# Kernel optimization log

Measured on AMD Instinct MI355X. Metric: run time of the kernel, lower is better.

The kernel has to match this reference:

```python
import jax, jax.numpy as jnp
import numpy as np

R = 29          # GF_kernel_size_train
EPS = 1e-09     # loss_eps
SAMPLING = 8    # sampling_in_MSEloss
LAMBDA_TV = 0.1
LAMBDA_HESSIAN = 0.5
ISO = True      # isotropic_hessian
SIGMA = 1.0     # hessian_kernel_sigma (>0.5 -> generateHessianKernel, angle_offset=[0])


def _hessian_kernels():
    half = int(np.ceil(SIGMA * 6))
    t = np.linspace(-half, half, 2 * half + 1)
    X, Y = np.meshgrid(t, t, indexing='ij')
    g = np.exp(-(X ** 2 + Y ** 2) / (2 * SIGMA ** 2))
    dxx = (1.0 / (2 * np.pi * SIGMA ** 4)) * (X ** 2 / SIGMA ** 2 - 1) * g
    dxy = (1.0 / (2 * np.pi * SIGMA ** 6)) * (X * Y) * g
    dyy = dxx.T
    # Loss.__init__ unpacks generateHessianKernel's return (Gaussyy, Gaussxx, Gaussxy)
    # into (self.DGaussxx, self.DGaussyy, self.DGaussxy); angle_offset=[0] -> identity rotate.
    Gxx = dyy.astype(np.float32)[None, None]
    Gyy = dxx.astype(np.float32)[None, None]
    Gxy = dxy.astype(np.float32)[None, None]
    return jnp.asarray(Gxx), jnp.asarray(Gyy), jnp.asarray(Gxy)


def _conv(x, k):
    return jax.lax.conv_general_dilated(x, k, (1, 1), 'VALID',
                                        dimension_numbers=('NCHW', 'OIHW', 'NCHW'))


def _boxfilter(x, r):
    # F.pad(input, (r+1, r, r+1, r)) pads last two dims (left r+1, right r each)
    xp = jnp.pad(x, ((0, 0), (0, 0), (r + 1, r), (r + 1, r)))
    c = jnp.cumsum(xp, axis=3)
    d = c[:, :, :, 2 * r + 1:] - c[:, :, :, :-2 * r - 1]
    c2 = jnp.cumsum(d, axis=2)
    return c2[:, :, 2 * r + 1:, :] - c2[:, :, :-2 * r - 1, :]


def _guided_filter(x, y, r, eps):
    N = _boxfilter(jnp.ones_like(x), r)
    mean_x = _boxfilter(x, r) / N
    mean_y = _boxfilter(y, r) / N
    cov_xy = _boxfilter(x * y, r) / N - mean_x * mean_y
    var_x = _boxfilter(x * x, r) / N - mean_x * mean_x
    A = cov_xy / jnp.clip(var_x, EPS, None)
    b = mean_y - A * mean_x
    A = _boxfilter(A, r) / N
    b = _boxfilter(b, r) / N
    return A * x + b


def _tv(x, target, Dx, Dy):
    return jnp.abs(_conv(x, Dx)).sum() + jnp.abs(_conv(x - target, Dy)).sum()


def _hessian(x, target, Gxx, Gyy, Gxy):
    scale = 2.0 if ISO else 1.0
    return (jnp.abs(_conv(x, Gxx)).sum()
            + jnp.abs(_conv(x - target, Gyy)).sum()
            + (jnp.abs(_conv(x - target, Gxy)) * scale).sum())


def setup_inputs() -> dict:
    key = jax.random.key(0)
    ks = jax.random.split(key, 6)
    shape = (1, 1, 3072, 3072)
    Gxx, Gyy, Gxy = _hessian_kernels()
    return {
        'outputGNNraw': jax.random.normal(ks[0], shape, dtype=jnp.float32),
        'outputGNN': jax.random.normal(ks[1], shape, dtype=jnp.float32),
        'outputLR': jax.random.normal(ks[2], shape, dtype=jnp.float32),
        'smoothedTarget': jax.random.normal(ks[3], shape, dtype=jnp.float32),
        'targets': jax.random.normal(ks[4], shape, dtype=jnp.float32),
        'map': jax.random.uniform(ks[5], shape, dtype=jnp.float32),
        'Dx': jnp.array([[1.0, -1.0]], dtype=jnp.float32)[None, None],   # [1,1,1,2]
        'Dy': jnp.array([[1.0], [-1.0]], dtype=jnp.float32)[None, None], # [1,1,2,1]
        'DGaussxx': Gxx, 'DGaussyy': Gyy, 'DGaussxy': Gxy,
    }


def reference(outputGNNraw, outputGNN, outputLR, smoothedTarget, targets, map,
              Dx, Dy, DGaussxx, DGaussyy, DGaussxy):
    gf = _guided_filter(outputGNNraw, outputGNNraw, R, EPS)
    mse = (jnp.abs(smoothedTarget - gf).sum()
           + (jnp.abs(targets - outputGNN) * map)[:, :, ::SAMPLING, ::SAMPLING].sum())
    tv = _tv(outputGNN, targets, Dx, Dy) + _tv(outputLR, targets, Dx, Dy)
    hess = (_hessian(outputGNN, targets, DGaussxx, DGaussyy, DGaussxy)
            + _hessian(outputLR, targets, DGaussxx, DGaussyy, DGaussxy))
    return mse + LAMBDA_TV * tv + LAMBDA_HESSIAN * hess
```

## Files before the change

kernel.cpp:

```cpp
#include <hip/hip_runtime.h>
#include <math.h>

#define W    3072
#define HH   3072
#define HOUT 3060
#define TW   64
#define TH   56
#define XR   68
#define XTS  76
#define VTS  77
#define VTW  (14*VTS)
#define GX   48
#define GY   55
#define GZ   2
#define NTHR (GX*GY*GZ*256)
#define NSLOT 64

struct HessTaps { float a[13]; float bb[13]; float m[13]; float n[13]; };

__device__ __forceinline__ void reduce_add(float v, double* a) {
  __shared__ float red[8];
  #pragma unroll
  for (int o = 32; o > 0; o >>= 1) v += __shfl_down(v, o, 64);
  int lane = threadIdx.x & 63, wid = threadIdx.x >> 6;
  if (lane == 0) red[wid] = v;
  __syncthreads();
  if (threadIdx.x == 0) {
    float s = red[0] + red[1] + red[2] + red[3];
    unsafeAtomicAdd(a, (double)s);
  }
  __syncthreads();
}

__global__ __launch_bounds__(256, 4) void hess_kernel(const float* __restrict__ Gnn,
                                                      const float* __restrict__ Lr,
                                                      const float* __restrict__ T,
                                                      const float* __restrict__ Xr,
                                                      const float* __restrict__ St,
                                                      const float* __restrict__ Mp,
                                                      double* acc, int slotmask,
                                                      HessTaps tp) {
  __shared__ float xt[XR * XTS];
  __shared__ float vt[4 * VTW];
  const float* img = (blockIdx.z == 0) ? Gnn : Lr;
  int oy = blockIdx.y * TH, ox = blockIdx.x * TW;
  int t = threadIdx.x;
  int wv = t >> 6, ln = t & 63;
  int r0 = wv * 14;

  for (int idx = t; idx < XR * 19; idx += 256) {
    int r = idx / 19, g = idx - r * 19;
    int gr = oy + r, gc = ox + 4 * g;
    float4 v = {0.f, 0.f, 0.f, 0.f};
    if (gr < HH) {
      const float* p = &img[(size_t)gr * W + gc];
      if (gc + 3 < W) v = *(const float4*)p;
      else {
        if (gc < W)     v.x = p[0];
        if (gc + 1 < W) v.y = p[1];
        if (gc + 2 < W) v.z = p[2];
      }
    }
    *(float4*)&xt[r * XTS + 4 * g] = v;
  }

  int bid = (blockIdx.z * GY + blockIdx.y) * GX + blockIdx.x;
  int i0 = bid * 256 + t;
  int i1 = i0 + NTHR;
  const int n4 = (W * HH) / 4;
  float4 ga0 = ((const float4*)Xr)[i0];
  float4 gb0 = ((const float4*)St)[i0];
  float4 ga1 = {0.f, 0.f, 0.f, 0.f}, gb1 = ga1;
  bool has1 = (i1 < n4);
  if (has1) { ga1 = ((const float4*)Xr)[i1]; gb1 = ((const float4*)St)[i1]; }
  float mT = 0.f, mG = 0.f, mM = 0.f;
  bool hasm = (i0 < 384 * 384);
  if (hasm) {
    int si = i0 / 384, sj = i0 - si * 384;
    int id = si * 8 * W + sj * 8;
    mT = T[id]; mG = Gnn[id]; mM = Mp[id];
  }
  __builtin_amdgcn_sched_barrier(0);

  __syncthreads();

  float tvl = 0.f;
  float hl  = 0.f;

  {
    int gc = ox + ln;
    if (gc < W - 1) {
      #pragma unroll
      for (int i = 0; i < 14; ++i) {
        int r = r0 + i;
        if (oy + r < HH)
          tvl += fabsf(xt[r * XTS + ln] - xt[r * XTS + ln + 1]);
      }
    }
  }

  #define VPASS(TAP)                                                        \
    {                                                                       \
       \
      float oA[14];                                                         \
      _Pragma("unroll")                                                     \
      for (int i = 0; i < 14; ++i) oA[i] = 0.f;                             \
      _Pragma("unroll")                                                     \
      for (int u = 0; u < 26; ++u) {                                        \
        float xA = xt[(r0 + u) * XTS + ln];                                 \
        _Pragma("unroll")                                                   \
        for (int i = 0; i < 14; ++i) {                                      \
          int kk = u - i;                                                   \
          if (kk >= 0 && kk <= 12) oA[i] = fmaf((TAP)[kk], xA, oA[i]);      \
        }                                                                   \
      }                                                                     \
      float* vw = &vt[wv * VTW + ln];                                       \
      _Pragma("unroll")                                                     \
      for (int i = 0; i < 14; ++i) vw[i * VTS] = oA[i];                     \
        \
      _Pragma("unroll")                                                     \
      for (int k = 0; k < 3; ++k) {                                         \
        int o = ln + 64 * k;                                                \
        if (o < 168) {                                                      \
          int row = o / 12, hc = o - row * 12;                              \
          const float* xp = &xt[(r0 + row) * XTS + 64 + hc];                \
          float s = 0.f;                                                    \
          _Pragma("unroll")                                                 \
          for (int u = 0; u < 13; ++u) s = fmaf((TAP)[u], xp[u * XTS], s);  \
          vt[wv * VTW + row * VTS + 64 + hc] = s;                           \
        }                                                                   \
      }                                                                     \
    }

  #define HSECOND(TAP, WGT)                                                 \
    {                                                                       \
      int r14 = ln & 15, cg = ln >> 4;                                      \
      if (r14 < 14) {                                                       \
        const float* vrow = &vt[wv * VTW + r14 * VTS + cg * 16];            \
        float o_[16];                                                       \
        _Pragma("unroll")                                                   \
        for (int jj = 0; jj < 16; ++jj) o_[jj] = 0.f;                       \
        _Pragma("unroll")                                                   \
        for (int j = 0; j < 28; ++j) {                                      \
          float v = vrow[j];                                                \
          _Pragma("unroll")                                                 \
          for (int jj = 0; jj < 16; ++jj) {                                 \
            int kk = j - jj;                                                \
            if (kk >= 0 && kk <= 12) o_[jj] = fmaf((TAP)[kk], v, o_[jj]);   \
          }                                                                 \
        }                                                                   \
        int gr = oy + r0 + r14;                                             \
        int gc0 = ox + cg * 16;                                             \
        float wr = (gr < HOUT) ? (WGT) : 0.f;                               \
        _Pragma("unroll")                                                   \
        for (int jj = 0; jj < 16; ++jj) {                                   \
          float m_ = (gc0 + jj < HOUT) ? wr : 0.f;                          \
          hl = fmaf(m_, fabsf(o_[jj]), hl);                                 \
        }                                                                   \
      }                                                                     \
    }

  VPASS(tp.bb);
  HSECOND(tp.a, 1.0f);

  __syncthreads();
  for (int idx = t; idx < XR * 19; idx += 256) {
    int r = idx / 19, g = idx - r * 19;
    int gr = oy + r, gc = ox + 4 * g;
    float4 v = {0.f, 0.f, 0.f, 0.f};
    if (gr < HH) {
      const float* p = &T[(size_t)gr * W + gc];
      if (gc + 3 < W) v = *(const float4*)p;
      else {
        if (gc < W)     v.x = p[0];
        if (gc + 1 < W) v.y = p[1];
        if (gc + 2 < W) v.z = p[2];
      }
    }
    float4 cur = *(float4*)&xt[r * XTS + 4 * g];
    cur.x -= v.x; cur.y -= v.y; cur.z -= v.z; cur.w -= v.w;
    *(float4*)&xt[r * XTS + 4 * g] = cur;
  }
  __syncthreads();

  {
    int gc = ox + ln;
    if (gc < W) {
      #pragma unroll
      for (int i = 0; i < 14; ++i) {
        int r = r0 + i;
        if (oy + r < HH - 1)
          tvl += fabsf(xt[r * XTS + ln] - xt[(r + 1) * XTS + ln]);
      }
    }
  }

  VPASS(tp.a);
  HSECOND(tp.bb, 1.0f);

  VPASS(tp.m);
  HSECOND(tp.n, 2.0f);

  float gm = fabsf(gb0.x - ga0.x) + fabsf(gb0.y - ga0.y)
           + fabsf(gb0.z - ga0.z) + fabsf(gb0.w - ga0.w);
  if (has1)
    gm += fabsf(gb1.x - ga1.x) + fabsf(gb1.y - ga1.y)
        + fabsf(gb1.z - ga1.z) + fabsf(gb1.w - ga1.w);
  if (hasm) gm += fabsf(mT - mG) * mM;

  int slot = bid & slotmask;
  double* base = acc + (size_t)slot * 32;
  reduce_add(gm,  base);
  reduce_add(tvl, base + 8);
  reduce_add(hl,  base + 16);
}

__global__ void finalize_kernel(const double* acc, int slotmask, float* out) {
  double s0 = 0.0, s1 = 0.0, s3 = 0.0;
  for (int s = 0; s <= slotmask; ++s) {
    s0 += acc[s * 32];
    s1 += acc[s * 32 + 8];
    s3 += acc[s * 32 + 16];
  }
  out[0] = (float)(s0 + 0.1 * s1 + 0.5 * s3);
}

extern "C" void kernel_launch(void* const* d_in, const int* in_sizes, int n_in,
                              void* d_out, int out_size, void* d_ws, size_t ws_size,
                              hipStream_t stream) {
  const float* xraw = (const float*)d_in[0];
  const float* gnn  = (const float*)d_in[1];
  const float* lr   = (const float*)d_in[2];
  const float* st   = (const float*)d_in[3];
  const float* tg   = (const float*)d_in[4];
  const float* mp   = (const float*)d_in[5];
  float* out = (float*)d_out;

  int nslot = NSLOT;
  while (nslot > 1 && (size_t)nslot * 256 > ws_size) nslot >>= 1;
  int slotmask = nslot - 1;

  double* acc = (double*)d_ws;
  hipMemsetAsync(d_ws, 0, (size_t)nslot * 256, stream);

  HessTaps tp;
  const double PI2 = 6.283185307179586476925287;
  for (int k = 0; k < 13; ++k) {
    double tt = (double)(k - 6);
    double g = exp(-0.5 * tt * tt);
    tp.a[k]  = (float)((tt * tt - 1.0) * g / PI2);
    tp.bb[k] = (float)g;
    tp.m[k]  = (float)(tt * g / PI2);
    tp.n[k]  = (float)(tt * g);
  }

  hess_kernel<<<dim3(GX, GY, GZ), 256, 0, stream>>>(gnn, lr, tg, xraw, st, mp,
                                                    acc, slotmask, tp);

  finalize_kernel<<<1, 1, 0, stream>>>(acc, slotmask, out);
}
```

Measured before the change: 285.8 us.

## Shrink tile height and prefetch target tile into registers early

```diff
diff --git a/kernel.cpp b/kernel.cpp
--- a/kernel.cpp
+++ b/kernel.cpp
@@ -5,16 +5,18 @@
 #define HH   3072
 #define HOUT 3060
 #define TW   64
-#define TH   56
-#define XR   68
+#define TH   44
+#define RW   11
+#define XR   56
 #define XTS  76
 #define VTS  77
-#define VTW  (14*VTS)
+#define VTW  (RW*VTS)
 #define GX   48
-#define GY   55
+#define GY   70
 #define GZ   2
 #define NTHR (GX*GY*GZ*256)
 #define NSLOT 64
+#define NSTG ((XR*19+255)/256)
 
 struct HessTaps { float a[13]; float bb[13]; float m[13]; float n[13]; };
 
@@ -32,7 +34,7 @@
   __syncthreads();
 }
 
-__global__ __launch_bounds__(256, 4) void hess_kernel(const float* __restrict__ Gnn,
+__global__ __launch_bounds__(256, 5) void hess_kernel(const float* __restrict__ Gnn,
                                                       const float* __restrict__ Lr,
                                                       const float* __restrict__ T,
                                                       const float* __restrict__ Xr,
@@ -46,7 +48,7 @@
   int oy = blockIdx.y * TH, ox = blockIdx.x * TW;
   int t = threadIdx.x;
   int wv = t >> 6, ln = t & 63;
-  int r0 = wv * 14;
+  int r0 = wv * RW;
 
   for (int idx = t; idx < XR * 19; idx += 256) {
     int r = idx / 19, g = idx - r * 19;
@@ -62,6 +64,27 @@
       }
     }
     *(float4*)&xt[r * XTS + 4 * g] = v;
+  }
+
+  float4 tr4[NSTG];
+  #pragma unroll
+  for (int k = 0; k < NSTG; ++k) {
+    int idx = t + 256 * k;
+    float4 v = {0.f, 0.f, 0.f, 0.f};
+    if (idx < XR * 19) {
+      int r = idx / 19, g = idx - r * 19;
+      int gr = oy + r, gc = ox + 4 * g;
+      if (gr < HH) {
+        const float* p = &T[(size_t)gr * W + gc];
+        if (gc + 3 < W) v = *(const float4*)p;
+        else {
+          if (gc < W)     v.x = p[0];
+          if (gc + 1 < W) v.y = p[1];
+          if (gc + 2 < W) v.z = p[2];
+        }
+      }
+    }
+    tr4[k] = v;
   }
 
   int bid = (blockIdx.z * GY + blockIdx.y) * GX + blockIdx.x;
@@ -91,7 +114,7 @@
     int gc = ox + ln;
     if (gc < W - 1) {
       #pragma unroll
-      for (int i = 0; i < 14; ++i) {
+      for (int i = 0; i < RW; ++i) {
         int r = r0 + i;
         if (oy + r < HH)
           tvl += fabsf(xt[r * XTS + ln] - xt[r * XTS + ln + 1]);
@@ -102,26 +125,26 @@
   #define VPASS(TAP)                                                        \
     {                                                                       \
        \
-      float oA[14];                                                         \
-      _Pragma("unroll")                                                     \
-      for (int i = 0; i < 14; ++i) oA[i] = 0.f;                             \
-      _Pragma("unroll")                                                     \
-      for (int u = 0; u < 26; ++u) {                                        \
+      float oA[RW];                                                         \
+      _Pragma("unroll")                                                     \
+      for (int i = 0; i < RW; ++i) oA[i] = 0.f;                             \
+      _Pragma("unroll")                                                     \
+      for (int u = 0; u < RW + 12; ++u) {                                   \
         float xA = xt[(r0 + u) * XTS + ln];                                 \
         _Pragma("unroll")                                                   \
-        for (int i = 0; i < 14; ++i) {                                      \
+        for (int i = 0; i < RW; ++i) {                                      \
           int kk = u - i;                                                   \
           if (kk >= 0 && kk <= 12) oA[i] = fmaf((TAP)[kk], xA, oA[i]);      \
         }                                                                   \
       }                                                                     \
       float* vw = &vt[wv * VTW + ln];                                       \
       _Pragma("unroll")                                                     \
-      for (int i = 0; i < 14; ++i) vw[i * VTS] = oA[i];                     \
-        \
+      for (int i = 0; i < RW; ++i) vw[i * VTS] = oA[i];                     \
+                   \
       _Pragma("unroll")                                                     \
       for (int k = 0; k < 3; ++k) {                                         \
         int o = ln + 64 * k;                                                \
-        if (o < 168) {                                                      \
+        if (o < 12 * RW) {                                                  \
           int row = o / 12, hc = o - row * 12;                              \
           const float* xp = &xt[(r0 + row) * XTS + 64 + hc];                \
           float s = 0.f;                                                    \
@@ -135,7 +158,7 @@
   #define HSECOND(TAP, WGT)                                                 \
     {                                                                       \
       int r14 = ln & 15, cg = ln >> 4;                                      \
-      if (r14 < 14) {                                                       \
+      if (r14 < RW) {                                                       \
         const float* vrow = &vt[wv * VTW + r14 * VTS + cg * 16];            \
         float o_[16];                                                       \
         _Pragma("unroll")                                                   \
@@ -164,22 +187,16 @@
   HSECOND(tp.a, 1.0f);
 
   __syncthreads();
-  for (int idx = t; idx < XR * 19; idx += 256) {
-    int r = idx / 19, g = idx - r * 19;
-    int gr = oy + r, gc = ox + 4 * g;
-    float4 v = {0.f, 0.f, 0.f, 0.f};
-    if (gr < HH) {
-      const float* p = &T[(size_t)gr * W + gc];
-      if (gc + 3 < W) v = *(const float4*)p;
-      else {
-        if (gc < W)     v.x = p[0];
-        if (gc + 1 < W) v.y = p[1];
-        if (gc + 2 < W) v.z = p[2];
-      }
-    }
-    float4 cur = *(float4*)&xt[r * XTS + 4 * g];
-    cur.x -= v.x; cur.y -= v.y; cur.z -= v.z; cur.w -= v.w;
-    *(float4*)&xt[r * XTS + 4 * g] = cur;
+  #pragma unroll
+  for (int k = 0; k < NSTG; ++k) {
+    int idx = t + 256 * k;
+    if (idx < XR * 19) {
+      int r = idx / 19, g = idx - r * 19;
+      float4 cur = *(float4*)&xt[r * XTS + 4 * g];
+      cur.x -= tr4[k].x; cur.y -= tr4[k].y;
+      cur.z -= tr4[k].z; cur.w -= tr4[k].w;
+      *(float4*)&xt[r * XTS + 4 * g] = cur;
+    }
   }
   __syncthreads();
 
@@ -187,7 +204,7 @@
     int gc = ox + ln;
     if (gc < W) {
       #pragma unroll
-      for (int i = 0; i < 14; ++i) {
+      for (int i = 0; i < RW; ++i) {
         int r = r0 + i;
         if (oy + r < HH - 1)
           tvl += fabsf(xt[r * XTS + ln] - xt[(r + 1) * XTS + ln]);
```

New measurement: 273.9 us. 4.1% less time.
